# Kernel tuning notes

Hardware: AMD Instinct MI355X
Metric: run time of the kernel (lower is better)

Reference implementation:

```python
import jax, jax.numpy as jnp
import numpy as np

DECAY = 0.99
EPS = 1e-5  # Laplace smoothing eps in cluster-size balancing


def _quantize(z_flat, embedding, cluster_size, emb_avg, n_codes):
    # z_flat: [N, D]; embedding: [K, D]
    d = (jnp.sum(z_flat * z_flat, axis=1, keepdims=True)
         + jnp.sum(embedding * embedding, axis=1)
         - 2.0 * (z_flat @ embedding.T))                      # [N, K]
    idx = jnp.argmin(d, axis=1)                               # [N]
    # EMA update (training path). segment_sum == one-hot matmul scatter-add.
    counts = jax.ops.segment_sum(jnp.ones(z_flat.shape[0], z_flat.dtype), idx,
                                 num_segments=n_codes)        # [K]
    new_cs = cluster_size * DECAY + (1.0 - DECAY) * counts
    dw = jax.ops.segment_sum(z_flat, idx, num_segments=n_codes)  # [K, D]
    new_avg = emb_avg * DECAY + (1.0 - DECAY) * dw
    n = new_cs.sum()
    bal = (new_cs + EPS) / (n + n_codes * EPS) * n
    # torch assigns via .data (no autograd) -> stop_gradient for faithfulness
    new_emb = jax.lax.stop_gradient(new_avg / bal[:, None])
    z_q = jnp.take(new_emb, idx, axis=0)  # == one_hot(idx) @ new_emb
    return idx, z_q


def _l2norm(x):
    # F.normalize(x, dim=-1) with eps=1e-12
    return x / jnp.maximum(jnp.linalg.norm(x, axis=-1, keepdims=True), 1e-12)


def reference(z, structure_embedding, style_embedding,
              structure_cluster_size, style_cluster_size,
              structure_embedding_avg, style_embedding_avg):
    b, c, h, w, d = z.shape
    zp = jnp.transpose(z, (0, 2, 3, 4, 1))      # b h w d c
    z_flat = zp.reshape(-1, c)                  # [N, D]
    s_idx, s_q = _quantize(z_flat, structure_embedding, structure_cluster_size,
                           structure_embedding_avg, structure_embedding.shape[0])
    y_idx, y_q = _quantize(z_flat, style_embedding, style_cluster_size,
                           style_embedding_avg, style_embedding.shape[0])

    def back(q):  # [N, C] -> b c h w d
        return jnp.transpose(q.reshape(b, h, w, d, c), (0, 4, 1, 2, 3))

    s_enc = back(s_q)
    y_enc = back(y_q)
    # NOTE: faithful to source — normalize over LAST axis of (b,c,h,w,d),
    # i.e. the spatial depth axis, exactly as F.normalize(dim=-1) does there.
    dis = jnp.mean(jnp.sum(_l2norm(s_enc) * _l2norm(y_enc), axis=-1) ** 2)
    z_q = (s_enc + y_enc) * 0.5
    return z_q, dis, s_idx, y_idx


def setup_inputs() -> dict:
    key = jax.random.key(0)
    k1, k2, k3 = jax.random.split(key, 3)
    B, C, H, W, D = 16, 256, 16, 16, 16
    Ks, Ky = 1024, 512
    return {
        "z": jax.random.normal(k1, (B, C, H, W, D), dtype=jnp.float32),
        "structure_embedding": jax.random.normal(k2, (Ks, C), dtype=jnp.float32),
        "style_embedding": jax.random.normal(k3, (Ky, C), dtype=jnp.float32),
        "structure_cluster_size": jnp.zeros((Ks,), jnp.float32),
        "style_cluster_size": jnp.zeros((Ky,), jnp.float32),
        "structure_embedding_avg": jnp.zeros((Ks, C), jnp.float32),
        "style_embedding_avg": jnp.zeros((Ky, C), jnp.float32),
    }
```

## Files before the change

### kernel.cpp

```cpp
#include <hip/hip_runtime.h>
#include <float.h>

#define NROWS 65536
#define CDIM  256
#define KS    1024
#define KY    512
#define KTOT  1536
#define SPB   4096

#define WB_CNT_S       0
#define WB_CNT_Y       4096
#define WB_RESCUE_CNT  6144
#define WB_DISACC      6152
#define WB_DW_S        6400
#define WB_DW_Y        1054976
#define WB_ZERO_BYTES  1579264
#define WB_EIMG        1579264
#define WB_EN2         2365696
#define WB_IDXS_I      2371840
#define WB_IDXY_I      2633984
#define WB_RLIST_S     2896128
#define WB_RLIST_Y     3158272
#define WB_BASE_S      3420416
#define WB_BASE_Y      3424512
#define WB_CUR_S       3426560
#define WB_CUR_Y       3430656
#define WB_SCALE_S     3432704
#define WB_SCALE_Y     3436800
#define WB_PERM_S      3438848
#define WB_PERM_Y      3700992
#define WB_KSORT_S     3963136
#define WB_KSORT_Y     4225280
#define WB_EMB_S       4487424
#define WB_EMB_Y       5536000

#define OFF_OUT_ZQ   0
#define OFF_OUT_DIS  16777216
#define OFF_OUT_SIDX 16777217
#define OFF_OUT_YIDX 16842753

typedef __attribute__((ext_vector_type(8)))  _Float16 f16x8;
typedef __attribute__((ext_vector_type(4)))  float    f32x4;

__device__ __forceinline__ unsigned int umn(unsigned int a, unsigned int b) { return a < b ? a : b; }
__device__ __forceinline__ unsigned int umx(unsigned int a, unsigned int b) { return a > b ? a : b; }

__global__ void prep_e(const float* __restrict__ Es, const float* __restrict__ Ey,
                       unsigned short* __restrict__ eimg, float* __restrict__ en2) {
    int k = blockIdx.x;
    int lane = threadIdx.x;
    const float* E = (k < KS) ? (Es + (size_t)k * CDIM) : (Ey + (size_t)(k - KS) * CDIM);
    float4 v = *(const float4*)(E + lane * 4);
    float nrm = v.x * v.x + v.y * v.y + v.z * v.z + v.w * v.w;
#pragma unroll
    for (int off = 32; off > 0; off >>= 1) nrm += __shfl_down(nrm, off);
    if (lane == 0) en2[k] = nrm;

    unsigned short q0 = __builtin_bit_cast(unsigned short, (_Float16)v.x);
    unsigned short q1 = __builtin_bit_cast(unsigned short, (_Float16)v.y);
    unsigned short q2 = __builtin_bit_cast(unsigned short, (_Float16)v.z);
    unsigned short q3 = __builtin_bit_cast(unsigned short, (_Float16)v.w);
    uint2 hp = make_uint2((unsigned)q0 | ((unsigned)q1 << 16),
                          (unsigned)q2 | ((unsigned)q3 << 16));

    int c0 = lane * 4;
    int kc = c0 >> 5, g = (c0 >> 3) & 3, j0 = c0 & 7;
    size_t byteoff = (size_t)(k >> 4) * 8192 + (size_t)kc * 1024
                   + (size_t)(g * 16 + (k & 15)) * 16 + (size_t)j0 * 2;
    *(uint2*)((char*)eimg + byteoff) = hp;
}

__global__ void prep_z(const float* __restrict__ z, float* __restrict__ zf) {
    __shared__ float Zs[32][257];
    int blk = blockIdx.x;
    int n0 = blk * 32, b = n0 >> 12, s0 = n0 & 4095;
    int t = threadIdx.x;
    const float* zb = z + (size_t)b * CDIM * SPB + s0;
#pragma unroll
    for (int i = 0; i < 32; ++i) {
        int l = i * 256 + t;
        int c = l >> 5, s = l & 31;
        Zs[s][c] = zb[(size_t)c * SPB + s];
    }
    __syncthreads();
#pragma unroll
    for (int j = 0; j < 8; ++j) {
        int gid = j * 256 + t;
        int nl = gid >> 6, fg = gid & 63;
        float4 v = *(const float4*)(&Zs[nl][fg * 4]);
        *(float4*)(&zf[(size_t)(n0 + nl) * 256 + fg * 4]) = v;
    }
}

#define LOADB(Bd, t_)                                                          \
    {                                                                          \
        const char* gb = (const char*)eimg + (size_t)(t_) * 8192 + lane16;     \
        _Pragma("unroll")                                                      \
        for (int kc = 0; kc < 8; ++kc)                                         \
            Bd[kc] = *(const f16x8*)(gb + kc * 1024);                          \
    }

#define COMPUTE(Bd, t_)                                                        \
    {                                                                          \
        f32x4 acc0 = {}, acc1 = {};                                            \
        _Pragma("unroll")                                                      \
        for (int kc = 0; kc < 8; ++kc) {                                       \
            acc0 = __builtin_amdgcn_mfma_f32_16x16x32_f16(A[0][kc], Bd[kc], acc0, 0, 0, 0); \
            acc1 = __builtin_amdgcn_mfma_f32_16x16x32_f16(A[1][kc], Bd[kc], acc1, 0, 0, 0); \
        }                                                                      \
        const int kcode = (t_) * 16 + (lane & 15);                             \
        const float en0 = en2[kcode] + 512.0f;                                 \
        const unsigned int tag = (unsigned int)kcode;                          \
        _Pragma("unroll")                                                      \
        for (int q = 0; q < 4; ++q) {                                          \
            float d0 = fmaf(-2.f, acc0[q], en0);                               \
            unsigned int du0 = (__float_as_uint(d0) & 0xFFFFF800u) | tag;      \
            m2a[0][q] = umn(m2a[0][q], umx(m1a[0][q], du0));                   \
            m1a[0][q] = umn(m1a[0][q], du0);                                   \
            float d1 = fmaf(-2.f, acc1[q], en0);                               \
            unsigned int du1 = (__float_as_uint(d1) & 0xFFFFF800u) | tag;      \
            m2a[1][q] = umn(m2a[1][q], umx(m1a[1][q], du1));                   \
            m1a[1][q] = umn(m1a[1][q], du1);                                   \
        }                                                                      \
    }

#define FLUSH(book, fo, io, cb, rl)                                            \
    {                                                                          \
        _Pragma("unroll")                                                      \
        for (int rg = 0; rg < 2; ++rg)                                         \
        _Pragma("unroll")                                                      \
        for (int q = 0; q < 4; ++q) {                                          \
            unsigned int v1 = m1a[rg][q], v2 = m2a[rg][q];                     \
            _Pragma("unroll")                                                  \
            for (int m = 8; m >= 1; m >>= 1) {                                 \
                unsigned int o1 = (unsigned int)__shfl_xor((int)v1, m);        \
                unsigned int o2 = (unsigned int)__shfl_xor((int)v2, m);        \
                v2 = umn(umn(v2, o2), umx(v1, o1));                            \
                v1 = umn(v1, o1);                                              \
            }                                                                  \
            if ((lane & 15) == 0) {                                            \
                int kw = (int)(v1 & 0x7FFu) - ((book) ? KS : 0);               \
                int n = n0 + rg * 16 + (lane >> 4) * 4 + q;                    \
                fo[n] = (float)kw;                                             \
                io[n] = kw;                                                    \
                atomicAdd(&cb[kw], 1);                                         \
                if ((v1 >> 11) + 4 > (v2 >> 11)) {                             \
                    int k2w = (int)(v2 & 0x7FFu) - ((book) ? KS : 0);          \
                    int pp = atomicAdd(&rescue_cnt[book], 1);                  \
                    if (pp < 65536) rl[pp] = n | (k2w << 16);                  \
                }                                                              \
            }                                                                  \
            m1a[rg][q] = 0xFFFFFFFFu; m2a[rg][q] = 0xFFFFFFFFu;                \
        }                                                                      \
    }

__launch_bounds__(256, 2)
__global__ void assign_kernel(const float* __restrict__ zf, const unsigned short* __restrict__ eimg,
                              const float* __restrict__ en2,
                              float* __restrict__ sidx_f, float* __restrict__ yidx_f,
                              int* __restrict__ sidx_i, int* __restrict__ yidx_i,
                              int* __restrict__ cnt_s, int* __restrict__ cnt_y,
                              int* __restrict__ rescue_cnt,
                              int* __restrict__ rlist_s, int* __restrict__ rlist_y) {
    const int tid = threadIdx.x, wave = tid >> 6, lane = tid & 63;
    const int n0 = blockIdx.x * 128 + wave * 32;
    const size_t lane16 = (size_t)(lane * 16);

    f16x8 A[2][8];
#pragma unroll
    for (int rg = 0; rg < 2; ++rg) {
        const float* zr = zf + (size_t)(n0 + rg * 16 + (lane & 15)) * 256 + (lane >> 4) * 8;
#pragma unroll
        for (int kc = 0; kc < 8; ++kc) {
            float4 f0 = *(const float4*)(zr + kc * 32);
            float4 f1 = *(const float4*)(zr + kc * 32 + 4);
            f16x8 a;
            a[0] = (_Float16)f0.x; a[1] = (_Float16)f0.y;
            a[2] = (_Float16)f0.z; a[3] = (_Float16)f0.w;
            a[4] = (_Float16)f1.x; a[5] = (_Float16)f1.y;
            a[6] = (_Float16)f1.z; a[7] = (_Float16)f1.w;
            A[rg][kc] = a;
        }
    }

    unsigned int m1a[2][4], m2a[2][4];
#pragma unroll
    for (int rg = 0; rg < 2; ++rg)
#pragma unroll
        for (int q = 0; q < 4; ++q) { m1a[rg][q] = 0xFFFFFFFFu; m2a[rg][q] = 0xFFFFFFFFu; }

    f16x8 B0[8], B1[8];
    LOADB(B0, 0);

#pragma unroll 1
    for (int t = 0; t < 64; t += 2) {
        LOADB(B1, t + 1);
        COMPUTE(B0, t);
        LOADB(B0, t + 2);
        COMPUTE(B1, t + 1);
    }
    FLUSH(0, sidx_f, sidx_i, cnt_s, rlist_s);

#pragma unroll 1
    for (int t = 64; t < 96; t += 2) {
        LOADB(B1, t + 1);
        COMPUTE(B0, t);
        if (t + 2 < 96) LOADB(B0, t + 2);
        COMPUTE(B1, t + 1);
    }
    FLUSH(1, yidx_f, yidx_i, cnt_y, rlist_y);
}

__global__ void rescue2_kernel(const float* __restrict__ zf,
                               const float* __restrict__ Es, const float* __restrict__ Ey,
                               const float* __restrict__ en2, const int* __restrict__ rcnt,
                               const int* __restrict__ rlist_s, const int* __restrict__ rlist_y,
                               float* __restrict__ sidx_f, float* __restrict__ yidx_f,
                               int* __restrict__ sidx_i, int* __restrict__ yidx_i,
                               int* __restrict__ cnt_s, int* __restrict__ cnt_y) {
    int cs = rcnt[0]; if (cs > 65536) cs = 65536;
    int cy = rcnt[1]; if (cy > 65536) cy = 65536;
    int total = cs + cy;
    const int lane = threadIdx.x & 63;
    const int nw = (gridDim.x * blockDim.x) >> 6;
    for (int e = (int)((blockIdx.x * blockDim.x + threadIdx.x) >> 6); e < total; e += nw) {
        int book = (e >= cs);
        unsigned int ent = (unsigned int)(book ? rlist_y[e - cs] : rlist_s[e]);
        int n  = (int)(ent & 0xFFFFu);
        int k2 = (int)(ent >> 16);
        int* idx_i = book ? yidx_i : sidx_i;
        float* idx_f = book ? yidx_f : sidx_f;
        int* cnt = book ? cnt_y : cnt_s;
        const float* E = book ? Ey : Es;
        const float* en2k = book ? (en2 + KS) : en2;
        int k1 = idx_i[n];
        float4 zv = *(const float4*)(zf + (size_t)n * 256 + lane * 4);
        float4 a  = *(const float4*)(E + (size_t)k1 * 256 + lane * 4);
        float4 c  = *(const float4*)(E + (size_t)k2 * 256 + lane * 4);
        float d1 = zv.x * a.x + zv.y * a.y + zv.z * a.z + zv.w * a.w;
        float d2 = zv.x * c.x + zv.y * c.y + zv.z * c.z + zv.w * c.w;
#pragma unroll
        for (int off = 32; off > 0; off >>= 1) {
            d1 += __shfl_down(d1, off);
            d2 += __shfl_down(d2, off);
        }
        if (lane == 0) {
            float dist1 = en2k[k1] - 2.f * d1;
            float dist2 = en2k[k2] - 2.f * d2;
            int nk = (dist2 < dist1 || (dist2 == dist1 && k2 < k1)) ? k2 : k1;
            if (nk != k1) {
                atomicSub(&cnt[k1], 1);
                atomicAdd(&cnt[nk], 1);
                idx_i[n] = nk;
                idx_f[n] = (float)nk;
            }
        }
    }
}

__global__ void scanbal_kernel(const float* __restrict__ cs_in, const float* __restrict__ cy_in,
                               const int* __restrict__ cnt_s, const int* __restrict__ cnt_y,
                               int* __restrict__ base_s, int* __restrict__ base_y,
                               int* __restrict__ cur_s, int* __restrict__ cur_y,
                               float* __restrict__ scale_s, float* __restrict__ scale_y) {
    __shared__ int   sc[1024];
    __shared__ float sf[1024];
    int K = blockIdx.x ? KY : KS;
    const float* csi = blockIdx.x ? cy_in : cs_in;
    const int*   cnt = blockIdx.x ? cnt_y : cnt_s;
    int* base = blockIdx.x ? base_y : base_s;
    int* cur  = blockIdx.x ? cur_y  : cur_s;
    float* scale = blockIdx.x ? scale_y : scale_s;
    int t = threadIdx.x;
    int c = (t < K) ? cnt[t] : 0;
    float ncs = (t < K) ? (csi[t] * 0.99f + 0.01f * (float)c) : 0.f;
    sc[t] = c;
    __syncthreads();
    for (int off = 1; off < 1024; off <<= 1) {
        int v = sc[t] + ((t >= off) ? sc[t - off] : 0);
        __syncthreads();
        sc[t] = v;
        __syncthreads();
    }
    int incl = sc[t];
    sf[t] = ncs;
    __syncthreads();
    for (int s2 = 512; s2 > 0; s2 >>= 1) {
        if (t < s2) sf[t] += sf[t + s2];
        __syncthreads();
    }
    float nsum = sf[0];
    if (t < K) {
        base[t] = incl - c;
        cur[t]  = incl - c;
        float bal = (ncs + 1e-5f) / (nsum + (float)K * 1e-5f) * nsum;
        scale[t] = 1.0f / bal;
    }
}

__global__ void scatter_kernel(const int* __restrict__ si, const int* __restrict__ yi,
                               int* __restrict__ cur_s, int* __restrict__ cur_y,
                               int* __restrict__ perm_s, int* __restrict__ perm_y,
                               int* __restrict__ ksort_s, int* __restrict__ ksort_y) {
    int i = blockIdx.x * 256 + threadIdx.x;
    if (i < NROWS) {
        int k = si[i]; int p = atomicAdd(&cur_s[k], 1);
        perm_s[p] = i; ksort_s[p] = k;
    } else {
        int n = i - NROWS; int k = yi[n]; int p = atomicAdd(&cur_y[k], 1);
        perm_y[p] = n; ksort_y[p] = k;
    }
}

__global__ void dw_kernel(const float* __restrict__ zf,
                          const int* __restrict__ perm_s, const int* __restrict__ ksort_s,
                          const int* __restrict__ perm_y, const int* __restrict__ ksort_y,
                          float* __restrict__ dw_s, float* __restrict__ dw_y) {
    __shared__ int keys[33];
    __shared__ int rows[32];
    const int t = threadIdx.x;
    int blk = blockIdx.x;
    const int* perm; const int* ks; float* dw; int p0;
    if (blk < NROWS / 32) { perm = perm_s; ks = ksort_s; dw = dw_s; p0 = blk * 32; }
    else                  { perm = perm_y; ks = ksort_y; dw = dw_y; p0 = (blk - NROWS / 32) * 32; }
    if (t < 32) { keys[t] = ks[p0 + t]; rows[t] = perm[p0 + t]; }
    if (t == 32) keys[32] = -1;
    __syncthreads();
    float acc = 0.f;
#pragma unroll 8
    for (int j = 0; j < 32; ++j) {
        acc += zf[(size_t)rows[j] * 256 + t];
        if (keys[j + 1] != keys[j]) {
            atomicAdd(&dw[(size_t)keys[j] * 256 + t], acc);
            acc = 0.f;
        }
    }
}

__global__ void embnew_kernel(const float* __restrict__ avg_s, const float* __restrict__ avg_y,
                              const float* __restrict__ dw_s, const float* __restrict__ dw_y,
                              const float* __restrict__ scale_s, const float* __restrict__ scale_y,
                              float* __restrict__ emb_s, float* __restrict__ emb_y) {
    int id = blockIdx.x, t = threadIdx.x;
    if (id < KS) { int i = id * 256 + t; emb_s[i] = (avg_s[i] * 0.99f + 0.01f * dw_s[i]) * scale_s[id]; }
    else { int kk = id - KS; int i = kk * 256 + t; emb_y[i] = (avg_y[i] * 0.99f + 0.01f * dw_y[i]) * scale_y[kk]; }
}

__global__ void gather_kernel(const float* __restrict__ Se, const float* __restrict__ Ye,
                              const int* __restrict__ sidx, const int* __restrict__ yidx,
                              float* __restrict__ zq, float* __restrict__ disacc) {
    __shared__ float qb[256 * 17];
    __shared__ int   si[16], yi[16];
    __shared__ float red[256];
    const int g  = blockIdx.x;
    const int b  = g >> 8;
    const int hw = g & 255;
    const int t  = threadIdx.x;
    if (t < 16) {
        int n = b * SPB + hw * 16 + t;
        si[t] = sidx[n];
        yi[t] = yidx[n];
    }
    __syncthreads();
    float ns = 0.f, ny = 0.f, dot = 0.f;
#pragma unroll
    for (int d = 0; d < 16; ++d) {
        float s = Se[(size_t)si[d] * CDIM + t];
        float y = Ye[(size_t)yi[d] * CDIM + t];
        ns  = fmaf(s, s, ns);
        ny  = fmaf(y, y, ny);
        dot = fmaf(s, y, dot);
        qb[t * 17 + d] = 0.5f * (s + y);
    }
    float den = fmaxf(sqrtf(ns), 1e-12f) * fmaxf(sqrtf(ny), 1e-12f);
    float val = dot / den;
    red[t] = val * val;
    __syncthreads();
    for (int s = 128; s > 0; s >>= 1) {
        if (t < s) red[t] += red[t + s];
        __syncthreads();
    }
    if (t == 0) atomicAdd(disacc, red[0]);
    float* zg = zq + (size_t)b * CDIM * SPB + hw * 16;
#pragma unroll
    for (int j = 0; j < 16; ++j) {
        int e = j * 256 + t;
        int c = e >> 4, d = e & 15;
        zg[(size_t)c * SPB + d] = qb[c * 17 + d];
    }
}

__global__ void fin_kernel(const float* __restrict__ disacc, float* __restrict__ out_dis) {
    *out_dis = *disacc * (1.0f / 1048576.0f);
}

extern "C" void kernel_launch(void* const* d_in, const int* in_sizes, int n_in,
                              void* d_out, int out_size, void* d_ws, size_t ws_size,
                              hipStream_t stream) {
    const float* z     = (const float*)d_in[0];
    const float* Es    = (const float*)d_in[1];
    const float* Ey    = (const float*)d_in[2];
    const float* s_cs  = (const float*)d_in[3];
    const float* y_cs  = (const float*)d_in[4];
    const float* s_avg = (const float*)d_in[5];
    const float* y_avg = (const float*)d_in[6];
    float* out = (float*)d_out;
    char*  w   = (char*)d_ws;

    unsigned short* eimg = (unsigned short*)(w + WB_EIMG);
    float* en2    = (float*)(w + WB_EN2);
    int* idxs_i   = (int*)(w + WB_IDXS_I);
    int* idxy_i   = (int*)(w + WB_IDXY_I);
    int* cnt_s    = (int*)(w + WB_CNT_S);
    int* cnt_y    = (int*)(w + WB_CNT_Y);
    int* r_cnt    = (int*)(w + WB_RESCUE_CNT);
    int* rlist_s  = (int*)(w + WB_RLIST_S);
    int* rlist_y  = (int*)(w + WB_RLIST_Y);
    int* base_s   = (int*)(w + WB_BASE_S);
    int* base_y   = (int*)(w + WB_BASE_Y);
    int* cur_s    = (int*)(w + WB_CUR_S);
    int* cur_y    = (int*)(w + WB_CUR_Y);
    float* scale_s = (float*)(w + WB_SCALE_S);
    float* scale_y = (float*)(w + WB_SCALE_Y);
    int* perm_s   = (int*)(w + WB_PERM_S);
    int* perm_y   = (int*)(w + WB_PERM_Y);
    int* ksort_s  = (int*)(w + WB_KSORT_S);
    int* ksort_y  = (int*)(w + WB_KSORT_Y);
    float* dw_s   = (float*)(w + WB_DW_S);
    float* dw_y   = (float*)(w + WB_DW_Y);
    float* emb_s  = (float*)(w + WB_EMB_S);
    float* emb_y  = (float*)(w + WB_EMB_Y);

    float* zf     = out + OFF_OUT_ZQ;
    float* sidx_f = out + OFF_OUT_SIDX;
    float* yidx_f = out + OFF_OUT_YIDX;

    hipMemsetAsync(w, 0, WB_ZERO_BYTES, stream);

    prep_e<<<KTOT, 64, 0, stream>>>(Es, Ey, eimg, en2);
    prep_z<<<NROWS / 32, 256, 0, stream>>>(z, zf);

    assign_kernel<<<NROWS / 128, 256, 0, stream>>>(zf, eimg, en2, sidx_f, yidx_f,
                                                   idxs_i, idxy_i, cnt_s, cnt_y,
                                                   r_cnt, rlist_s, rlist_y);

    rescue2_kernel<<<512, 256, 0, stream>>>(zf, Es, Ey, en2, r_cnt, rlist_s, rlist_y,
                                            sidx_f, yidx_f, idxs_i, idxy_i, cnt_s, cnt_y);

    scanbal_kernel<<<2, 1024, 0, stream>>>(s_cs, y_cs, cnt_s, cnt_y, base_s, base_y,
                                           cur_s, cur_y, scale_s, scale_y);
    scatter_kernel<<<2 * NROWS / 256, 256, 0, stream>>>(idxs_i, idxy_i, cur_s, cur_y,
                                                        perm_s, perm_y, ksort_s, ksort_y);
    dw_kernel<<<2 * NROWS / 32, 256, 0, stream>>>(zf, perm_s, ksort_s, perm_y, ksort_y, dw_s, dw_y);
    embnew_kernel<<<KTOT, 256, 0, stream>>>(s_avg, y_avg, dw_s, dw_y, scale_s, scale_y, emb_s, emb_y);
    gather_kernel<<<4096, 256, 0, stream>>>(emb_s, emb_y, idxs_i, idxy_i,
                                            out + OFF_OUT_ZQ, (float*)(w + WB_DISACC));
    fin_kernel<<<1, 1, 0, stream>>>((float*)(w + WB_DISACC), out + OFF_OUT_DIS);
}
```

Baseline: 316.1 us.

## Widen assign kernel to 64 rows per wave and prefetch code norms

Each wave now covers 64 rows (four 16-row MFMA groups) instead of 32, so every codebook B fragment loaded from global memory feeds twice as many MFMAs. Blocks shrink to 128 threads with launch bounds (128,1), and the two codebook loops are merged into one with a mid-loop flush. The en2 norm load moves into the prefetch stage, and sched_barriers pin the load/compute order. The cost is much higher register pressure from the doubled A fragments and accumulators, which may reduce occupancy or cause spills, and the grid keeps NROWS/128 blocks, so fewer waves are resident overall.

```diff
diff --git a/kernel.cpp b/kernel.cpp
--- a/kernel.cpp
+++ b/kernel.cpp
@@ -92,42 +92,51 @@
     }
 }
 
-#define LOADB(Bd, t_)                                                          \
+#define LOADB(Bd, en_, t_)                                                     \
     {                                                                          \
         const char* gb = (const char*)eimg + (size_t)(t_) * 8192 + lane16;     \
         _Pragma("unroll")                                                      \
         for (int kc = 0; kc < 8; ++kc)                                         \
             Bd[kc] = *(const f16x8*)(gb + kc * 1024);                          \
-    }
-
-#define COMPUTE(Bd, t_)                                                        \
+        en_ = en2[(t_) * 16 + (lane & 15)] + 512.0f;                           \
+    }
+
+#define COMPUTE(Bd, en_, t_)                                                   \
     {                                                                          \
-        f32x4 acc0 = {}, acc1 = {};                                            \
+        f32x4 acc0 = {}, acc1 = {}, acc2 = {}, acc3 = {};                      \
         _Pragma("unroll")                                                      \
         for (int kc = 0; kc < 8; ++kc) {                                       \
             acc0 = __builtin_amdgcn_mfma_f32_16x16x32_f16(A[0][kc], Bd[kc], acc0, 0, 0, 0); \
             acc1 = __builtin_amdgcn_mfma_f32_16x16x32_f16(A[1][kc], Bd[kc], acc1, 0, 0, 0); \
+            acc2 = __builtin_amdgcn_mfma_f32_16x16x32_f16(A[2][kc], Bd[kc], acc2, 0, 0, 0); \
+            acc3 = __builtin_amdgcn_mfma_f32_16x16x32_f16(A[3][kc], Bd[kc], acc3, 0, 0, 0); \
         }                                                                      \
-        const int kcode = (t_) * 16 + (lane & 15);                             \
-        const float en0 = en2[kcode] + 512.0f;                                 \
-        const unsigned int tag = (unsigned int)kcode;                          \
+        const unsigned int tag = (unsigned int)((t_) * 16 + (lane & 15));      \
         _Pragma("unroll")                                                      \
         for (int q = 0; q < 4; ++q) {                                          \
-            float d0 = fmaf(-2.f, acc0[q], en0);                               \
+            float d0 = fmaf(-2.f, acc0[q], en_);                               \
             unsigned int du0 = (__float_as_uint(d0) & 0xFFFFF800u) | tag;      \
             m2a[0][q] = umn(m2a[0][q], umx(m1a[0][q], du0));                   \
             m1a[0][q] = umn(m1a[0][q], du0);                                   \
-            float d1 = fmaf(-2.f, acc1[q], en0);                               \
+            float d1 = fmaf(-2.f, acc1[q], en_);                               \
             unsigned int du1 = (__float_as_uint(d1) & 0xFFFFF800u) | tag;      \
             m2a[1][q] = umn(m2a[1][q], umx(m1a[1][q], du1));                   \
             m1a[1][q] = umn(m1a[1][q], du1);                                   \
+            float d2 = fmaf(-2.f, acc2[q], en_);                               \
+            unsigned int du2 = (__float_as_uint(d2) & 0xFFFFF800u) | tag;      \
+            m2a[2][q] = umn(m2a[2][q], umx(m1a[2][q], du2));                   \
+            m1a[2][q] = umn(m1a[2][q], du2);                                   \
+            float d3 = fmaf(-2.f, acc3[q], en_);                               \
+            unsigned int du3 = (__float_as_uint(d3) & 0xFFFFF800u) | tag;      \
+            m2a[3][q] = umn(m2a[3][q], umx(m1a[3][q], du3));                   \
+            m1a[3][q] = umn(m1a[3][q], du3);                                   \
         }                                                                      \
     }
 
 #define FLUSH(book, fo, io, cb, rl)                                            \
     {                                                                          \
         _Pragma("unroll")                                                      \
-        for (int rg = 0; rg < 2; ++rg)                                         \
+        for (int rg = 0; rg < 4; ++rg)                                         \
         _Pragma("unroll")                                                      \
         for (int q = 0; q < 4; ++q) {                                          \
             unsigned int v1 = m1a[rg][q], v2 = m2a[rg][q];                     \
@@ -154,7 +163,7 @@
         }                                                                      \
     }
 
-__launch_bounds__(256, 2)
+__launch_bounds__(128, 1)
 __global__ void assign_kernel(const float* __restrict__ zf, const unsigned short* __restrict__ eimg,
                               const float* __restrict__ en2,
                               float* __restrict__ sidx_f, float* __restrict__ yidx_f,
@@ -163,12 +172,12 @@
                               int* __restrict__ rescue_cnt,
                               int* __restrict__ rlist_s, int* __restrict__ rlist_y) {
     const int tid = threadIdx.x, wave = tid >> 6, lane = tid & 63;
-    const int n0 = blockIdx.x * 128 + wave * 32;
+    const int n0 = blockIdx.x * 128 + wave * 64;
     const size_t lane16 = (size_t)(lane * 16);
 
-    f16x8 A[2][8];
-#pragma unroll
-    for (int rg = 0; rg < 2; ++rg) {
+    f16x8 A[4][8];
+#pragma unroll
+    for (int rg = 0; rg < 4; ++rg) {
         const float* zr = zf + (size_t)(n0 + rg * 16 + (lane & 15)) * 256 + (lane >> 4) * 8;
 #pragma unroll
         for (int kc = 0; kc < 8; ++kc) {
@@ -183,30 +192,26 @@
         }
     }
 
-    unsigned int m1a[2][4], m2a[2][4];
-#pragma unroll
-    for (int rg = 0; rg < 2; ++rg)
+    unsigned int m1a[4][4], m2a[4][4];
+#pragma unroll
+    for (int rg = 0; rg < 4; ++rg)
 #pragma unroll
         for (int q = 0; q < 4; ++q) { m1a[rg][q] = 0xFFFFFFFFu; m2a[rg][q] = 0xFFFFFFFFu; }
 
     f16x8 B0[8], B1[8];
-    LOADB(B0, 0);
+    float enA, enB;
+    LOADB(B0, enA, 0);
+    __builtin_amdgcn_sched_barrier(0);
 
 #pragma unroll 1
-    for (int t = 0; t < 64; t += 2) {
-        LOADB(B1, t + 1);
-        COMPUTE(B0, t);
-        LOADB(B0, t + 2);
-        COMPUTE(B1, t + 1);
-    }
-    FLUSH(0, sidx_f, sidx_i, cnt_s, rlist_s);
-
-#pragma unroll 1
-    for (int t = 64; t < 96; t += 2) {
-        LOADB(B1, t + 1);
-        COMPUTE(B0, t);
-        if (t + 2 < 96) LOADB(B0, t + 2);
-        COMPUTE(B1, t + 1);
+    for (int t = 0; t < 96; t += 2) {
+        if (t + 1 < 96) LOADB(B1, enB, t + 1);
+        __builtin_amdgcn_sched_barrier(0);
+        COMPUTE(B0, enA, t);
+        if (t + 2 < 96) LOADB(B0, enA, t + 2);
+        __builtin_amdgcn_sched_barrier(0);
+        COMPUTE(B1, enB, t + 1);
+        if (t + 1 == 63) FLUSH(0, sidx_f, sidx_i, cnt_s, rlist_s);
     }
     FLUSH(1, yidx_f, yidx_i, cnt_y, rlist_y);
 }
@@ -440,7 +445,7 @@
     prep_e<<<KTOT, 64, 0, stream>>>(Es, Ey, eimg, en2);
     prep_z<<<NROWS / 32, 256, 0, stream>>>(z, zf);
 
-    assign_kernel<<<NROWS / 128, 256, 0, stream>>>(zf, eimg, en2, sidx_f, yidx_f,
+    assign_kernel<<<NROWS / 128, 128, 0, stream>>>(zf, eimg, en2, sidx_f, yidx_f,
                                                    idxs_i, idxy_i, cnt_s, cnt_y,
                                                    r_cnt, rlist_s, rlist_y);
 
```

New measurement: 338.7 us. +7.2%, slower.

## Triple-buffer codebook tile loads with inline asm and explicit vmcnt waits

Applied to the files above, without the earlier changes.

Replaces the double-buffered codebook loads in the fused distance/argmin kernel with a three-stage software pipeline. Each stage issues hand-written global_load_dwordx4 instructions plus the per-code norm load, and waits with an explicit s_waitcnt vmcnt, so two tiles stay in flight during each MFMA batch. The two codebook loops are merged into one, with the structure flush done at tile 63. s_setprio raises wave priority around the MFMA block. In exchange the compiler no longer tracks these loads, the vmcnt counts must be correct by hand, the extra buffer raises register pressure, and the last iteration prefetches past the final tile.

```diff
diff --git a/kernel.cpp b/kernel.cpp
--- a/kernel.cpp
+++ b/kernel.cpp
@@ -92,25 +92,43 @@
     }
 }
 
-#define LOADB(Bd, t_)                                                          \
+#define LOADB(Bd, en_, t_)                                                     \
     {                                                                          \
-        const char* gb = (const char*)eimg + (size_t)(t_) * 8192 + lane16;     \
-        _Pragma("unroll")                                                      \
-        for (int kc = 0; kc < 8; ++kc)                                         \
-            Bd[kc] = *(const f16x8*)(gb + kc * 1024);                          \
-    }
-
-#define COMPUTE(Bd, t_)                                                        \
+        const char* gb0 = (const char*)eimg + (size_t)(t_) * 8192 + lane16;    \
+        const char* gb1 = gb0 + 4096;                                          \
+        const char* ep  = (const char*)en2 + (size_t)(((t_) << 4) + (lane & 15)) * 4; \
+        asm volatile(                                                          \
+            "global_load_dwordx4 %0, %8, off\n\t"                              \
+            "global_load_dwordx4 %1, %8, off offset:1024\n\t"                  \
+            "global_load_dwordx4 %2, %8, off offset:2048\n\t"                  \
+            "global_load_dwordx4 %3, %8, off offset:3072\n\t"                  \
+            "global_load_dwordx4 %4, %9, off\n\t"                              \
+            "global_load_dwordx4 %5, %9, off offset:1024\n\t"                  \
+            "global_load_dwordx4 %6, %9, off offset:2048\n\t"                  \
+            "global_load_dwordx4 %7, %9, off offset:3072"                      \
+            : "=v"(Bd[0]), "=v"(Bd[1]), "=v"(Bd[2]), "=v"(Bd[3]),              \
+              "=v"(Bd[4]), "=v"(Bd[5]), "=v"(Bd[6]), "=v"(Bd[7])               \
+            : "v"(gb0), "v"(gb1));                                             \
+        asm volatile("global_load_dword %0, %1, off" : "=v"(en_) : "v"(ep));   \
+    }
+
+#define WAITP(n)                                                               \
+    asm volatile("s_waitcnt vmcnt(" #n ")");                                   \
+    __builtin_amdgcn_sched_barrier(0);
+
+#define COMPUTE(Bd, en_, t_)                                                   \
     {                                                                          \
         f32x4 acc0 = {}, acc1 = {};                                            \
+        __builtin_amdgcn_s_setprio(1);                                         \
         _Pragma("unroll")                                                      \
         for (int kc = 0; kc < 8; ++kc) {                                       \
-            acc0 = __builtin_amdgcn_mfma_f32_16x16x32_f16(A[0][kc], Bd[kc], acc0, 0, 0, 0); \
-            acc1 = __builtin_amdgcn_mfma_f32_16x16x32_f16(A[1][kc], Bd[kc], acc1, 0, 0, 0); \
+            f16x8 Bf = __builtin_bit_cast(f16x8, Bd[kc]);                      \
+            acc0 = __builtin_amdgcn_mfma_f32_16x16x32_f16(A[0][kc], Bf, acc0, 0, 0, 0); \
+            acc1 = __builtin_amdgcn_mfma_f32_16x16x32_f16(A[1][kc], Bf, acc1, 0, 0, 0); \
         }                                                                      \
-        const int kcode = (t_) * 16 + (lane & 15);                             \
-        const float en0 = en2[kcode] + 512.0f;                                 \
-        const unsigned int tag = (unsigned int)kcode;                          \
+        __builtin_amdgcn_s_setprio(0);                                         \
+        const float en0 = en_ + 512.0f;                                        \
+        const unsigned int tag = (unsigned int)(((t_) << 4) + (lane & 15));    \
         _Pragma("unroll")                                                      \
         for (int q = 0; q < 4; ++q) {                                          \
             float d0 = fmaf(-2.f, acc0[q], en0);                               \
@@ -189,24 +207,24 @@
 #pragma unroll
         for (int q = 0; q < 4; ++q) { m1a[rg][q] = 0xFFFFFFFFu; m2a[rg][q] = 0xFFFFFFFFu; }
 
-    f16x8 B0[8], B1[8];
-    LOADB(B0, 0);
+    f32x4 B0[8], B1[8], B2[8];
+    float en0v, en1v, en2v;
+
+    LOADB(B0, en0v, 0);
+    LOADB(B1, en1v, 1);
 
 #pragma unroll 1
-    for (int t = 0; t < 64; t += 2) {
-        LOADB(B1, t + 1);
-        COMPUTE(B0, t);
-        LOADB(B0, t + 2);
-        COMPUTE(B1, t + 1);
-    }
-    FLUSH(0, sidx_f, sidx_i, cnt_s, rlist_s);
-
-#pragma unroll 1
-    for (int t = 64; t < 96; t += 2) {
-        LOADB(B1, t + 1);
-        COMPUTE(B0, t);
-        if (t + 2 < 96) LOADB(B0, t + 2);
-        COMPUTE(B1, t + 1);
+    for (int T = 0; T < 96; T += 3) {
+        LOADB(B2, en2v, T + 2);
+        WAITP(18);
+        COMPUTE(B0, en0v, T);
+        if (T == 63) FLUSH(0, sidx_f, sidx_i, cnt_s, rlist_s);
+        LOADB(B0, en0v, T + 3);
+        WAITP(18);
+        COMPUTE(B1, en1v, T + 1);
+        LOADB(B1, en1v, T + 4);
+        WAITP(18);
+        COMPUTE(B2, en2v, T + 2);
     }
     FLUSH(1, yidx_f, yidx_i, cnt_y, rlist_y);
 }
```

Measured after the change: 309.6 us. 1.02x faster.

## Stage codebook tiles into LDS via async global_load_lds with 4-deep ring

Applied to the files above, without the earlier changes.

The assign kernel now copies codebook fp16 tiles into a shared 4-slot LDS ring with direct global-to-LDS loads, cooperatively across the four waves. Each wave then reads its MFMA B operands from LDS instead of loading the full codebook from global memory itself. The goal is to cut redundant per-wave global and L2 traffic and to overlap loads with compute through a prefetch two phases ahead. In exchange it adds 64KB of LDS per block, which may limit occupancy to one block per CU, a block barrier every phase, and hand-written vmcnt waits that must match the issued load count exactly.

```diff
diff --git a/kernel.cpp b/kernel.cpp
--- a/kernel.cpp
+++ b/kernel.cpp
@@ -92,37 +92,20 @@
     }
 }
 
-#define LOADB(Bd, t_)                                                          \
-    {                                                                          \
-        const char* gb = (const char*)eimg + (size_t)(t_) * 8192 + lane16;     \
-        _Pragma("unroll")                                                      \
-        for (int kc = 0; kc < 8; ++kc)                                         \
-            Bd[kc] = *(const f16x8*)(gb + kc * 1024);                          \
-    }
-
-#define COMPUTE(Bd, t_)                                                        \
-    {                                                                          \
-        f32x4 acc0 = {}, acc1 = {};                                            \
-        _Pragma("unroll")                                                      \
-        for (int kc = 0; kc < 8; ++kc) {                                       \
-            acc0 = __builtin_amdgcn_mfma_f32_16x16x32_f16(A[0][kc], Bd[kc], acc0, 0, 0, 0); \
-            acc1 = __builtin_amdgcn_mfma_f32_16x16x32_f16(A[1][kc], Bd[kc], acc1, 0, 0, 0); \
-        }                                                                      \
-        const int kcode = (t_) * 16 + (lane & 15);                             \
-        const float en0 = en2[kcode] + 512.0f;                                 \
-        const unsigned int tag = (unsigned int)kcode;                          \
-        _Pragma("unroll")                                                      \
-        for (int q = 0; q < 4; ++q) {                                          \
-            float d0 = fmaf(-2.f, acc0[q], en0);                               \
-            unsigned int du0 = (__float_as_uint(d0) & 0xFFFFF800u) | tag;      \
-            m2a[0][q] = umn(m2a[0][q], umx(m1a[0][q], du0));                   \
-            m1a[0][q] = umn(m1a[0][q], du0);                                   \
-            float d1 = fmaf(-2.f, acc1[q], en0);                               \
-            unsigned int du1 = (__float_as_uint(d1) & 0xFFFFF800u) | tag;      \
-            m2a[1][q] = umn(m2a[1][q], umx(m1a[1][q], du1));                   \
-            m1a[1][q] = umn(m1a[1][q], du1);                                   \
-        }                                                                      \
-    }
+__device__ __forceinline__ void stage_phase(const unsigned short* __restrict__ eimg,
+                                            int phase, char* lds, int wave, int lane) {
+    const char* gs = (const char*)eimg + (size_t)phase * 16384 + wave * 4096 + lane * 16;
+    char* ls = lds + wave * 4096;
+#pragma unroll
+    for (int i = 0; i < 4; ++i)
+        __builtin_amdgcn_global_load_lds(
+            (const __attribute__((address_space(1))) void*)(gs + i * 1024),
+            (__attribute__((address_space(3))) void*)(ls + i * 1024), 16, 0, 0);
+}
+
+#define WAITV(n)                                                               \
+    asm volatile("s_waitcnt vmcnt(" #n ")");                                   \
+    __builtin_amdgcn_sched_barrier(0);
 
 #define FLUSH(book, fo, io, cb, rl)                                            \
     {                                                                          \
@@ -162,9 +145,9 @@
                               int* __restrict__ cnt_s, int* __restrict__ cnt_y,
                               int* __restrict__ rescue_cnt,
                               int* __restrict__ rlist_s, int* __restrict__ rlist_y) {
+    __shared__ char sh[4][16384];
     const int tid = threadIdx.x, wave = tid >> 6, lane = tid & 63;
     const int n0 = blockIdx.x * 128 + wave * 32;
-    const size_t lane16 = (size_t)(lane * 16);
 
     f16x8 A[2][8];
 #pragma unroll
@@ -189,24 +172,46 @@
 #pragma unroll
         for (int q = 0; q < 4; ++q) { m1a[rg][q] = 0xFFFFFFFFu; m2a[rg][q] = 0xFFFFFFFFu; }
 
-    f16x8 B0[8], B1[8];
-    LOADB(B0, 0);
+    stage_phase(eimg, 0, &sh[0][0], wave, lane);
+    stage_phase(eimg, 1, &sh[1][0], wave, lane);
 
 #pragma unroll 1
-    for (int t = 0; t < 64; t += 2) {
-        LOADB(B1, t + 1);
-        COMPUTE(B0, t);
-        LOADB(B0, t + 2);
-        COMPUTE(B1, t + 1);
-    }
-    FLUSH(0, sidx_f, sidx_i, cnt_s, rlist_s);
-
-#pragma unroll 1
-    for (int t = 64; t < 96; t += 2) {
-        LOADB(B1, t + 1);
-        COMPUTE(B0, t);
-        if (t + 2 < 96) LOADB(B0, t + 2);
-        COMPUTE(B1, t + 1);
+    for (int p = 0; p < 48; ++p) {
+        if (p + 2 < 48) stage_phase(eimg, p + 2, &sh[(p + 2) & 3][0], wave, lane);
+        if (p < 46)       { WAITV(8); }
+        else if (p == 46) { WAITV(4); }
+        else              { WAITV(0); }
+        __builtin_amdgcn_s_barrier();
+        asm volatile("" ::: "memory");
+
+#pragma unroll
+        for (int c = 0; c < 2; ++c) {
+            const char* bb = &sh[p & 3][c * 8192] + lane * 16;
+            f32x4 acc0 = {}, acc1 = {};
+#pragma unroll
+            for (int kc = 0; kc < 8; ++kc) {
+                f16x8 B = *(const f16x8*)(bb + kc * 1024);
+                acc0 = __builtin_amdgcn_mfma_f32_16x16x32_f16(A[0][kc], B, acc0, 0, 0, 0);
+                acc1 = __builtin_amdgcn_mfma_f32_16x16x32_f16(A[1][kc], B, acc1, 0, 0, 0);
+            }
+            const int kcode = (2 * p + c) * 16 + (lane & 15);
+            const float en0 = en2[kcode] + 512.0f;
+            const unsigned int tag = (unsigned int)kcode;
+#pragma unroll
+            for (int q = 0; q < 4; ++q) {
+                float d0 = fmaf(-2.f, acc0[q], en0);
+                unsigned int du0 = (__float_as_uint(d0) & 0xFFFFF800u) | tag;
+                m2a[0][q] = umn(m2a[0][q], umx(m1a[0][q], du0));
+                m1a[0][q] = umn(m1a[0][q], du0);
+                float d1 = fmaf(-2.f, acc1[q], en0);
+                unsigned int du1 = (__float_as_uint(d1) & 0xFFFFF800u) | tag;
+                m2a[1][q] = umn(m2a[1][q], umx(m1a[1][q], du1));
+                m1a[1][q] = umn(m1a[1][q], du1);
+            }
+        }
+        asm volatile("" ::: "memory");
+
+        if (p == 31) FLUSH(0, sidx_f, sidx_i, cnt_s, rlist_s);
     }
     FLUSH(1, yidx_f, yidx_i, cnt_y, rlist_y);
 }
```

Measured after the change: 321.9 us. About the same (+1.9%).
